# Kernel optimization log

Measured on AMD Instinct MI355X. Metric: run time of the kernel, lower is better.

Reference implementation:

```python
import jax, jax.numpy as jnp
import numpy as np


def setup_inputs() -> dict:
    key = jax.random.key(0)
    k1, k2, k3, k4 = jax.random.split(key, 4)
    B, IN, OUT, S = 8192, 2048, 3072, 8
    scale = 1.0 / (IN ** 0.5)
    x = jax.random.normal(k1, (B, IN), dtype=jnp.float32)
    subject_ids = jax.random.randint(k2, (B,), 0, S, dtype=jnp.int64)
    weights = jax.random.normal(k3, (S, IN, OUT), dtype=jnp.float32) * scale
    bias = jax.random.normal(k4, (S, OUT), dtype=jnp.float32) * scale
    return {"x": x, "subject_ids": subject_ids, "weights": weights, "bias": bias}


def reference(x, subject_ids, weights, bias):
    # Math: out[b] = x[b] @ weights[subject_ids[b]] + bias[subject_ids[b]]
    # Avoid materializing the [B, in, out] gathered weight tensor:
    # contract via a one-hot subject selector instead (same math).
    S = weights.shape[0]
    onehot = jax.nn.one_hot(subject_ids, S, dtype=x.dtype)  # [B, S]
    # [B,d] x [S,d,o] x [B,S] -> [B,o]; intermediate is at most [B,S,o]
    out = jnp.einsum('bd,sdo,bs->bo', x, weights, onehot)
    out = out + bias[subject_ids]  # [B, out]
    return out
```

## Files before the change

kernel.cpp:

```cpp
#include <hip/hip_runtime.h>
#include <hip/hip_bf16.h>
#include <stdint.h>

#define B_ROWS 8192
#define K_DIM  2048
#define N_DIM  3072
#define S_NUM  8

#define BM 256
#define BN 256
#define BK 64
#define NT (K_DIM / BK)
#define MAX_T256 40

#define BMF 128
#define BNF 128
#define BKF 32
#define NKF (K_DIM / BKF)
#define MAX_TILES 72
#define LDA 40
#define LDB 40

typedef __bf16 bf16x8 __attribute__((ext_vector_type(8)));
typedef float  f32x4  __attribute__((ext_vector_type(4)));
typedef unsigned int   u32x4 __attribute__((ext_vector_type(4)));
typedef unsigned short u16x8 __attribute__((ext_vector_type(8)));

#define WS_CNT    0
#define WS_OFFS   256
#define WS_T256S  512
#define WS_T256M  768
#define WS_TILES  1024
#define WS_TILEM  1536
#define WS_RANK   4096
#define WS_PERM   36864
#define WS_XPERM  262144
#define WS_WT     34865152
#define WS_NEED   135528448ULL

__device__ __forceinline__ unsigned int f2bf_pk(float lo, float hi) {
#if __has_builtin(__builtin_amdgcn_cvt_pk_bf16_f32)
    typedef __bf16 bf16x2_t __attribute__((ext_vector_type(2)));
    bf16x2_t v = __builtin_amdgcn_cvt_pk_bf16_f32(lo, hi);
    return __builtin_bit_cast(unsigned int, v);
#else
    unsigned int a = __builtin_bit_cast(unsigned int, lo);
    unsigned int b = __builtin_bit_cast(unsigned int, hi);
    a += 0x7FFFu + ((a >> 16) & 1u);
    b += 0x7FFFu + ((b >> 16) & 1u);
    return (a >> 16) | (b & 0xFFFF0000u);
#endif
}

__device__ __forceinline__ void gl_lds16(const void* g, void* l) {
    __builtin_amdgcn_global_load_lds(
        (const __attribute__((address_space(1))) void*)g,
        (__attribute__((address_space(3))) void*)l, 16, 0, 0);
}

__global__ void zero_cnt_kernel(int* __restrict__ cnt) {
    if (threadIdx.x < S_NUM) cnt[threadIdx.x] = 0;
}

__global__ void bucket_kernel(const int* __restrict__ ids,
                              int* __restrict__ cnt,
                              unsigned short* __restrict__ perm,
                              int* __restrict__ rank) {
    const int b = blockIdx.x * blockDim.x + threadIdx.x;
    const int lane = threadIdx.x & 63;
    const int s = ids[b];
    #pragma unroll
    for (int sub = 0; sub < S_NUM; ++sub) {
        unsigned long long m = __ballot(s == sub);
        if (s == sub) {
            int prefix = __popcll(m & ((1ull << lane) - 1ull));
            int leader = __ffsll((unsigned long long)m) - 1;
            int base = 0;
            if (lane == leader) base = atomicAdd(&cnt[sub], __popcll(m));
            base = __shfl(base, leader);
            perm[sub * B_ROWS + base + prefix] = (unsigned short)b;
            rank[b] = base + prefix;
        }
    }
}

__global__ void plan_kernel(const int* __restrict__ cnt, int* __restrict__ offs,
                            int* __restrict__ t256s, int* __restrict__ t256m,
                            int* __restrict__ tfs, int* __restrict__ tfm) {
    if (threadIdx.x == 0 && blockIdx.x == 0) {
        int t = 0, tf = 0, o = 0;
        for (int s = 0; s < S_NUM; ++s) {
            offs[s] = o; o += cnt[s];
            for (int m0 = 0; m0 < cnt[s]; m0 += BM)  { t256s[t] = s; t256m[t] = m0; ++t; }
            for (int m0 = 0; m0 < cnt[s]; m0 += BMF) { tfs[tf] = s;  tfm[tf] = m0;  ++tf; }
        }
        for (; t < MAX_T256; ++t)    { t256s[t] = -1; t256m[t] = 0; }
        for (; tf < MAX_TILES; ++tf) { tfs[tf]  = -1; tfm[tf]  = 0; }
    }
}

__global__ void convert_x_kernel(const float* __restrict__ x,
                                 const int* __restrict__ ids,
                                 const int* __restrict__ rank,
                                 const int* __restrict__ offs,
                                 unsigned short* __restrict__ xq) {
    const int b = blockIdx.x;
    const int dst = offs[ids[b]] + rank[b];
    const float* src = x + (size_t)b * K_DIM + threadIdx.x * 8;
    f32x4 v0 = *(const f32x4*)(src + 0);
    f32x4 v1 = *(const f32x4*)(src + 4);
    u32x4 p = { f2bf_pk(v0[0], v0[1]), f2bf_pk(v0[2], v0[3]),
                f2bf_pk(v1[0], v1[1]), f2bf_pk(v1[2], v1[3]) };
    *(u32x4*)(xq + (size_t)dst * K_DIM + threadIdx.x * 8) = p;
}

#define TW_LD 136
__global__ void convert_w_kernel(const float* __restrict__ w,
                                 unsigned short* __restrict__ wt) {
    const int kt = blockIdx.x, nt = blockIdx.y, s = blockIdx.z;
    __shared__ __align__(16) unsigned short lds[32 * TW_LD];

    const int tid = threadIdx.x;
    {
        const int k = tid >> 3;
        const int nseg = tid & 7;
        const float* src = w + ((size_t)s * K_DIM + kt * 32 + k) * N_DIM
                             + nt * 128 + nseg * 16;
        f32x4 v0 = *(const f32x4*)(src + 0);
        f32x4 v1 = *(const f32x4*)(src + 4);
        f32x4 v2 = *(const f32x4*)(src + 8);
        f32x4 v3 = *(const f32x4*)(src + 12);
        u32x4 p0 = { f2bf_pk(v0[0], v0[1]), f2bf_pk(v0[2], v0[3]),
                     f2bf_pk(v1[0], v1[1]), f2bf_pk(v1[2], v1[3]) };
        u32x4 p1 = { f2bf_pk(v2[0], v2[1]), f2bf_pk(v2[2], v2[3]),
                     f2bf_pk(v3[0], v3[1]), f2bf_pk(v3[2], v3[3]) };
        *(u32x4*)&lds[k * TW_LD + nseg * 16 + 0] = p0;
        *(u32x4*)&lds[k * TW_LD + nseg * 16 + 8] = p1;
    }
    __syncthreads();
    {
        const int n = tid >> 1;
        const int half = tid & 1;
        u16x8 o0, o1;
        #pragma unroll
        for (int j = 0; j < 8; ++j) {
            o0[j] = lds[(half * 16 + j) * TW_LD + n];
            o1[j] = lds[(half * 16 + 8 + j) * TW_LD + n];
        }
        unsigned short* dst = wt + ((size_t)s * N_DIM + nt * 128 + n) * K_DIM
                                 + kt * 32 + half * 16;
        *(u16x8*)(dst + 0) = o0;
        *(u16x8*)(dst + 8) = o1;
    }
}

__global__ __launch_bounds__(512, 2)
void gemm256_kernel(const unsigned short* __restrict__ xq,
                    const unsigned short* __restrict__ wt,
                    const float* __restrict__ bias,
                    const int* __restrict__ cnt,
                    const int* __restrict__ offs,
                    const int* __restrict__ tile_s,
                    const int* __restrict__ tile_m,
                    const unsigned short* __restrict__ perm,
                    float* __restrict__ out) {
    const int s = tile_s[blockIdx.x];
    if (s < 0) return;
    const int row0 = tile_m[blockIdx.x];
    const int rows = min(BM, cnt[s] - row0);
    const int n0   = blockIdx.y * BN;

    __shared__ __align__(16) char smem[131072 + 1024];
    int* prow = (int*)(smem + 131072);

    const int tid = threadIdx.x;
    if (tid < BM) {
        int rr = (tid < rows) ? tid : (rows - 1);
        prow[tid] = (int)perm[s * B_ROWS + row0 + rr];
    }

    const int lane = tid & 63;
    const int w    = tid >> 6;
    const int wr   = w >> 2;
    const int wc   = w & 3;
    const int l15  = lane & 15;
    const int quad = lane >> 4;

    const int srow  = w * 8 + (lane >> 3);
    const int sperm = ((lane & 7) ^ (lane >> 3)) << 3;
    const int rowA0 = offs[s] + row0;
    const unsigned short* aSrc = xq + (size_t)(rowA0 + srow) * K_DIM + sperm;
    const unsigned short* bSrc = wt + ((size_t)s * N_DIM + n0 + srow) * K_DIM + sperm;
    char* const aDst = smem + w * 1024;
    char* const bDst = smem + 65536 + w * 1024;

    auto stageA = [&](int half, int tt, int bb) {
        int ttc = (tt < NT) ? tt : (NT - 1);
        const unsigned short* g = aSrc + (size_t)half * (128 * K_DIM) + ttc * BK;
        char* d = aDst + (bb * 2 + half) * 16384;
        gl_lds16(g, d);
        gl_lds16(g + 64 * K_DIM, d + 8192);
    };
    auto stageB = [&](int half, int tt, int bb) {
        int ttc = (tt < NT) ? tt : (NT - 1);
        const unsigned short* g = bSrc + (size_t)half * (128 * K_DIM) + ttc * BK;
        char* d = bDst + (bb * 2 + half) * 16384;
        gl_lds16(g, d);
        gl_lds16(g + 64 * K_DIM, d + 8192);
    };

    bf16x8 af[4][2], bfr[2][2];
    auto ldsA = [&](int mh, int bb) {
        const char* base = smem + (bb * 2 + wr) * 16384;
        #pragma unroll
        for (int mt = 0; mt < 4; ++mt) {
            const int row = mh * 64 + mt * 16 + l15;
            #pragma unroll
            for (int kk = 0; kk < 2; ++kk) {
                const int kb = ((kk * 4 + quad) ^ (l15 & 7)) << 4;
                af[mt][kk] = *(const bf16x8*)(base + row * 128 + kb);
            }
        }
    };
    auto ldsB = [&](int nh, int bb) {
        const char* base = smem + 65536 + (bb * 2 + (wc >> 1)) * 16384;
        #pragma unroll
        for (int nt = 0; nt < 2; ++nt) {
            const int row = (wc & 1) * 64 + nh * 32 + nt * 16 + l15;
            #pragma unroll
            for (int kk = 0; kk < 2; ++kk) {
                const int kb = ((kk * 4 + quad) ^ (l15 & 7)) << 4;
                bfr[nt][kk] = *(const bf16x8*)(base + row * 128 + kb);
            }
        }
    };

    f32x4 acc[8][4] = {};
    auto mmac = [&](int mh, int nh) {
        #pragma unroll
        for (int kk = 0; kk < 2; ++kk)
            #pragma unroll
            for (int mt = 0; mt < 4; ++mt)
                #pragma unroll
                for (int nt = 0; nt < 2; ++nt)
                    acc[mh * 4 + mt][nh * 2 + nt] =
                        __builtin_amdgcn_mfma_f32_16x16x32_bf16(
                            af[mt][kk], bfr[nt][kk],
                            acc[mh * 4 + mt][nh * 2 + nt], 0, 0, 0);
    };

    stageA(0, 0, 0); stageA(1, 0, 0);
    stageB(0, 0, 0); stageB(1, 0, 0);
    stageB(0, 1, 1);
    asm volatile("s_waitcnt vmcnt(2)" ::: "memory");
    __builtin_amdgcn_s_barrier();

    for (int T = 0; T < NT; ++T) {
        const int bb = T & 1, nb = bb ^ 1;
        ldsA(0, bb); ldsB(0, bb);
        stageB(1, T + 1, nb);
        __builtin_amdgcn_s_barrier();
        __builtin_amdgcn_s_setprio(1);
        mmac(0, 0);
        __builtin_amdgcn_s_setprio(0);
        __builtin_amdgcn_s_barrier();
        ldsA(1, bb);
        stageA(0, T + 1, nb);
        __builtin_amdgcn_s_barrier();
        __builtin_amdgcn_s_setprio(1);
        mmac(1, 0);
        __builtin_amdgcn_s_setprio(0);
        __builtin_amdgcn_s_barrier();
        ldsB(1, bb);
        stageA(1, T + 1, nb);
        __builtin_amdgcn_s_barrier();
        __builtin_amdgcn_s_setprio(1);
        mmac(1, 1);
        __builtin_amdgcn_s_setprio(0);
        __builtin_amdgcn_s_barrier();
        ldsA(0, bb);
        stageB(0, T + 2, bb);
        asm volatile("s_waitcnt vmcnt(2)" ::: "memory");
        __builtin_amdgcn_s_barrier();
        __builtin_amdgcn_s_setprio(1);
        mmac(0, 1);
        __builtin_amdgcn_s_setprio(0);
        __builtin_amdgcn_s_barrier();
    }

    asm volatile("s_waitcnt vmcnt(0)" ::: "memory");

    float bvals[4];
    #pragma unroll
    for (int nt = 0; nt < 4; ++nt)
        bvals[nt] = bias[s * N_DIM + n0 + wc * 64 + nt * 16 + l15];

    #pragma unroll
    for (int mt = 0; mt < 8; ++mt) {
        #pragma unroll
        for (int r = 0; r < 4; ++r) {
            const int rl = wr * 128 + mt * 16 + quad * 4 + r;
            if (rl < rows) {
                float* op = out + (size_t)prow[rl] * N_DIM + n0 + wc * 64 + l15;
                #pragma unroll
                for (int nt = 0; nt < 4; ++nt)
                    op[nt * 16] = acc[mt][nt][r] + bvals[nt];
            }
        }
    }
}

__global__ __launch_bounds__(256, 3)
void subject_gemm_fb(const float* __restrict__ x,
                     const float* __restrict__ w,
                     const float* __restrict__ bias,
                     const int* __restrict__ cnt,
                     const int* __restrict__ tile_s,
                     const int* __restrict__ tile_m,
                     const unsigned short* __restrict__ perm,
                     float* __restrict__ out) {
    const int s = tile_s[blockIdx.x];
    if (s < 0) return;
    const int row0 = tile_m[blockIdx.x];
    const int rows = min(BMF, cnt[s] - row0);
    const int n0   = blockIdx.y * BNF;

    __shared__ __align__(16) unsigned short sA[BMF * LDA];
    __shared__ __align__(16) unsigned short sB[BNF * LDB];
    __shared__ int prow[BMF];

    const int tid = threadIdx.x;
    if (tid < BMF) {
        int rr = (tid < rows) ? tid : (rows - 1);
        prow[tid] = (int)perm[s * B_ROWS + row0 + rr];
    }
    __syncthreads();

    const int ar = tid >> 1;
    const int ah = tid & 1;
    const float* xp = x + (size_t)prow[ar] * K_DIM + ah * 16;
    const int bn  = tid & 127;
    const int bk2 = tid >> 7;
    const float* wp = w + (size_t)s * ((size_t)K_DIM * N_DIM)
                        + (size_t)(bk2 * 16) * N_DIM + (n0 + bn);

    const int lane = tid & 63;
    const int wid  = tid >> 6;
    const int wm   = (wid >> 1) * 64;
    const int wn   = (wid & 1) * 64;
    const int l15  = lane & 15;
    const int quad = lane >> 4;

    f32x4 acc[4][4] = {};
    f32x4 a0, a1, a2, a3;
    float bv[16];
    {
        a0 = *(const f32x4*)(xp + 0);  a1 = *(const f32x4*)(xp + 4);
        a2 = *(const f32x4*)(xp + 8);  a3 = *(const f32x4*)(xp + 12);
        #pragma unroll
        for (int i = 0; i < 16; ++i) bv[i] = wp[(size_t)i * N_DIM];
    }

    for (int ks = 0; ks < NKF; ++ks) {
        u32x4 pa0 = { f2bf_pk(a0[0],a0[1]), f2bf_pk(a0[2],a0[3]),
                      f2bf_pk(a1[0],a1[1]), f2bf_pk(a1[2],a1[3]) };
        u32x4 pa1 = { f2bf_pk(a2[0],a2[1]), f2bf_pk(a2[2],a2[3]),
                      f2bf_pk(a3[0],a3[1]), f2bf_pk(a3[2],a3[3]) };
        u32x4 pb0 = { f2bf_pk(bv[0],bv[1]),   f2bf_pk(bv[2],bv[3]),
                      f2bf_pk(bv[4],bv[5]),   f2bf_pk(bv[6],bv[7]) };
        u32x4 pb1 = { f2bf_pk(bv[8],bv[9]),   f2bf_pk(bv[10],bv[11]),
                      f2bf_pk(bv[12],bv[13]), f2bf_pk(bv[14],bv[15]) };

        __syncthreads();
        *(u32x4*)&sA[ar * LDA + ah * 16 + 0] = pa0;
        *(u32x4*)&sA[ar * LDA + ah * 16 + 8] = pa1;
        *(u32x4*)&sB[bn * LDB + bk2 * 16 + 0] = pb0;
        *(u32x4*)&sB[bn * LDB + bk2 * 16 + 8] = pb1;
        __syncthreads();

        if (ks + 1 < NKF) {
            const float* xq2 = xp + (ks + 1) * BKF;
            a0 = *(const f32x4*)(xq2 + 0);  a1 = *(const f32x4*)(xq2 + 4);
            a2 = *(const f32x4*)(xq2 + 8);  a3 = *(const f32x4*)(xq2 + 12);
            const float* wq = wp + (size_t)((ks + 1) * BKF) * N_DIM;
            #pragma unroll
            for (int i = 0; i < 16; ++i) bv[i] = wq[(size_t)i * N_DIM];
        }

        bf16x8 af[4], bfr[4];
        #pragma unroll
        for (int mt = 0; mt < 4; ++mt)
            af[mt] = *(const bf16x8*)&sA[(wm + mt * 16 + l15) * LDA + quad * 8];
        #pragma unroll
        for (int nt = 0; nt < 4; ++nt)
            bfr[nt] = *(const bf16x8*)&sB[(wn + nt * 16 + l15) * LDB + quad * 8];

        #pragma unroll
        for (int mt = 0; mt < 4; ++mt)
            #pragma unroll
            for (int nt = 0; nt < 4; ++nt)
                acc[mt][nt] = __builtin_amdgcn_mfma_f32_16x16x32_bf16(
                    af[mt], bfr[nt], acc[mt][nt], 0, 0, 0);
    }

    float bvals[4];
    #pragma unroll
    for (int nt = 0; nt < 4; ++nt)
        bvals[nt] = bias[s * N_DIM + n0 + wn + nt * 16 + l15];
    #pragma unroll
    for (int mt = 0; mt < 4; ++mt) {
        #pragma unroll
        for (int r = 0; r < 4; ++r) {
            int rl = wm + mt * 16 + quad * 4 + r;
            if (rl < rows) {
                float* op = out + (size_t)prow[rl] * N_DIM + n0 + wn + l15;
                #pragma unroll
                for (int nt = 0; nt < 4; ++nt)
                    op[nt * 16] = acc[mt][nt][r] + bvals[nt];
            }
        }
    }
}

extern "C" void kernel_launch(void* const* d_in, const int* in_sizes, int n_in,
                              void* d_out, int out_size, void* d_ws, size_t ws_size,
                              hipStream_t stream) {
    const float* x    = (const float*)d_in[0];
    const int*   sid  = (const int*)d_in[1];
    const float* w    = (const float*)d_in[2];
    const float* bias = (const float*)d_in[3];
    float* out = (float*)d_out;

    char* ws = (char*)d_ws;
    int* cnt    = (int*)(ws + WS_CNT);
    int* offs   = (int*)(ws + WS_OFFS);
    int* t256s  = (int*)(ws + WS_T256S);
    int* t256m  = (int*)(ws + WS_T256M);
    int* tfs    = (int*)(ws + WS_TILES);
    int* tfm    = (int*)(ws + WS_TILEM);
    int* rank   = (int*)(ws + WS_RANK);
    unsigned short* perm = (unsigned short*)(ws + WS_PERM);

    hipLaunchKernelGGL(zero_cnt_kernel, dim3(1), dim3(64), 0, stream, cnt);
    hipLaunchKernelGGL(bucket_kernel, dim3(B_ROWS / 256), dim3(256), 0, stream,
                       sid, cnt, perm, rank);
    hipLaunchKernelGGL(plan_kernel, dim3(1), dim3(64), 0, stream,
                       cnt, offs, t256s, t256m, tfs, tfm);

    if (ws_size >= WS_NEED) {
        unsigned short* xq = (unsigned short*)(ws + WS_XPERM);
        unsigned short* wt = (unsigned short*)(ws + WS_WT);
        hipLaunchKernelGGL(convert_x_kernel, dim3(B_ROWS), dim3(256), 0, stream,
                           x, sid, rank, offs, xq);
        hipLaunchKernelGGL(convert_w_kernel, dim3(K_DIM / 32, N_DIM / 128, S_NUM),
                           dim3(256), 0, stream, w, wt);
        dim3 grid(MAX_T256, N_DIM / BN);
        hipLaunchKernelGGL(gemm256_kernel, grid, dim3(512), 0, stream,
                           xq, wt, bias, cnt, offs, t256s, t256m, perm, out);
    } else {
        dim3 grid(MAX_TILES, N_DIM / BNF);
        hipLaunchKernelGGL(subject_gemm_fb, grid, dim3(256), 0, stream,
                           x, w, bias, cnt, tfs, tfm, perm, out);
    }
}
```

Baseline: 519.6 us.

## Fuse bucketing prep kernels and reorder GEMM inner loop to double-buffer B fragments

Three small setup kernels (zero counts, bucket rows by subject, build tile plan) are merged into one single-block kernel that counts with LDS atomics, removing two launches and the global atomics. The GEMM main loop is reordered so B fragments for both N-halves sit in separate register sets (bf0/bf1). This lets each quarter step reuse the fragments already loaded and drops one A reload per K-tile. The cost is extra VGPR pressure and a serial single-block prep pass over all 8192 rows.

```diff
diff --git a/kernel.cpp b/kernel.cpp
--- a/kernel.cpp
+++ b/kernel.cpp
@@ -58,41 +58,43 @@
         (__attribute__((address_space(3))) void*)l, 16, 0, 0);
 }
 
-__global__ void zero_cnt_kernel(int* __restrict__ cnt) {
-    if (threadIdx.x < S_NUM) cnt[threadIdx.x] = 0;
-}
-
-__global__ void bucket_kernel(const int* __restrict__ ids,
-                              int* __restrict__ cnt,
-                              unsigned short* __restrict__ perm,
-                              int* __restrict__ rank) {
-    const int b = blockIdx.x * blockDim.x + threadIdx.x;
-    const int lane = threadIdx.x & 63;
-    const int s = ids[b];
+__global__ __launch_bounds__(1024)
+void prep_kernel(const int* __restrict__ ids,
+                 int* __restrict__ cnt, int* __restrict__ offs,
+                 int* __restrict__ t256s, int* __restrict__ t256m,
+                 int* __restrict__ tfs, int* __restrict__ tfm,
+                 unsigned short* __restrict__ perm, int* __restrict__ rank) {
+    __shared__ int lcnt[S_NUM];
+    const int tid = threadIdx.x;
+    if (tid < S_NUM) lcnt[tid] = 0;
+    __syncthreads();
+    const int lane = tid & 63;
     #pragma unroll
-    for (int sub = 0; sub < S_NUM; ++sub) {
-        unsigned long long m = __ballot(s == sub);
-        if (s == sub) {
-            int prefix = __popcll(m & ((1ull << lane) - 1ull));
-            int leader = __ffsll((unsigned long long)m) - 1;
-            int base = 0;
-            if (lane == leader) base = atomicAdd(&cnt[sub], __popcll(m));
-            base = __shfl(base, leader);
-            perm[sub * B_ROWS + base + prefix] = (unsigned short)b;
-            rank[b] = base + prefix;
-        }
-    }
-}
-
-__global__ void plan_kernel(const int* __restrict__ cnt, int* __restrict__ offs,
-                            int* __restrict__ t256s, int* __restrict__ t256m,
-                            int* __restrict__ tfs, int* __restrict__ tfm) {
-    if (threadIdx.x == 0 && blockIdx.x == 0) {
+    for (int c = 0; c < B_ROWS / 1024; ++c) {
+        const int b = c * 1024 + tid;
+        const int s = ids[b];
+        #pragma unroll
+        for (int sub = 0; sub < S_NUM; ++sub) {
+            unsigned long long m = __ballot(s == sub);
+            if (s == sub) {
+                int prefix = __popcll(m & ((1ull << lane) - 1ull));
+                int leader = __ffsll((unsigned long long)m) - 1;
+                int base = 0;
+                if (lane == leader) base = atomicAdd(&lcnt[sub], __popcll(m));
+                base = __shfl(base, leader);
+                perm[sub * B_ROWS + base + prefix] = (unsigned short)b;
+                rank[b] = base + prefix;
+            }
+        }
+    }
+    __syncthreads();
+    if (tid == 0) {
         int t = 0, tf = 0, o = 0;
-        for (int s = 0; s < S_NUM; ++s) {
-            offs[s] = o; o += cnt[s];
-            for (int m0 = 0; m0 < cnt[s]; m0 += BM)  { t256s[t] = s; t256m[t] = m0; ++t; }
-            for (int m0 = 0; m0 < cnt[s]; m0 += BMF) { tfs[tf] = s;  tfm[tf] = m0;  ++tf; }
+        for (int s2 = 0; s2 < S_NUM; ++s2) {
+            const int c2 = lcnt[s2];
+            cnt[s2] = c2; offs[s2] = o; o += c2;
+            for (int m0 = 0; m0 < c2; m0 += BM)  { t256s[t] = s2; t256m[t] = m0; ++t; }
+            for (int m0 = 0; m0 < c2; m0 += BMF) { tfs[tf] = s2;  tfm[tf] = m0;  ++tf; }
         }
         for (; t < MAX_T256; ++t)    { t256s[t] = -1; t256m[t] = 0; }
         for (; tf < MAX_TILES; ++tf) { tfs[tf]  = -1; tfm[tf]  = 0; }
@@ -209,7 +211,7 @@
         gl_lds16(g + 64 * K_DIM, d + 8192);
     };
 
-    bf16x8 af[4][2], bfr[2][2];
+    bf16x8 af[4][2], bf0[2][2], bf1[2][2];
     auto ldsA = [&](int mh, int bb) {
         const char* base = smem + (bb * 2 + wr) * 16384;
         #pragma unroll
@@ -222,7 +224,7 @@
             }
         }
     };
-    auto ldsB = [&](int nh, int bb) {
+    auto ldsB = [&](int nh, int bb, bf16x8 (*dst)[2]) {
         const char* base = smem + 65536 + (bb * 2 + (wc >> 1)) * 16384;
         #pragma unroll
         for (int nt = 0; nt < 2; ++nt) {
@@ -230,13 +232,13 @@
             #pragma unroll
             for (int kk = 0; kk < 2; ++kk) {
                 const int kb = ((kk * 4 + quad) ^ (l15 & 7)) << 4;
-                bfr[nt][kk] = *(const bf16x8*)(base + row * 128 + kb);
+                dst[nt][kk] = *(const bf16x8*)(base + row * 128 + kb);
             }
         }
     };
 
     f32x4 acc[8][4] = {};
-    auto mmac = [&](int mh, int nh) {
+    auto mmac = [&](bf16x8 (*b)[2], int mh, int nh) {
         #pragma unroll
         for (int kk = 0; kk < 2; ++kk)
             #pragma unroll
@@ -245,7 +247,7 @@
                 for (int nt = 0; nt < 2; ++nt)
                     acc[mh * 4 + mt][nh * 2 + nt] =
                         __builtin_amdgcn_mfma_f32_16x16x32_bf16(
-                            af[mt][kk], bfr[nt][kk],
+                            af[mt][kk], b[nt][kk],
                             acc[mh * 4 + mt][nh * 2 + nt], 0, 0, 0);
     };
 
@@ -257,33 +259,32 @@
 
     for (int T = 0; T < NT; ++T) {
         const int bb = T & 1, nb = bb ^ 1;
-        ldsA(0, bb); ldsB(0, bb);
+        ldsA(0, bb); ldsB(0, bb, bf0);
         stageB(1, T + 1, nb);
         __builtin_amdgcn_s_barrier();
         __builtin_amdgcn_s_setprio(1);
-        mmac(0, 0);
+        mmac(bf0, 0, 0);
         __builtin_amdgcn_s_setprio(0);
         __builtin_amdgcn_s_barrier();
+        ldsB(1, bb, bf1);
+        stageA(0, T + 1, nb);
+        __builtin_amdgcn_s_barrier();
+        __builtin_amdgcn_s_setprio(1);
+        mmac(bf1, 0, 1);
+        __builtin_amdgcn_s_setprio(0);
+        __builtin_amdgcn_s_barrier();
         ldsA(1, bb);
-        stageA(0, T + 1, nb);
+        stageA(1, T + 1, nb);
         __builtin_amdgcn_s_barrier();
         __builtin_amdgcn_s_setprio(1);
-        mmac(1, 0);
+        mmac(bf1, 1, 1);
         __builtin_amdgcn_s_setprio(0);
         __builtin_amdgcn_s_barrier();
-        ldsB(1, bb);
-        stageA(1, T + 1, nb);
-        __builtin_amdgcn_s_barrier();
-        __builtin_amdgcn_s_setprio(1);
-        mmac(1, 1);
-        __builtin_amdgcn_s_setprio(0);
-        __builtin_amdgcn_s_barrier();
-        ldsA(0, bb);
         stageB(0, T + 2, bb);
         asm volatile("s_waitcnt vmcnt(2)" ::: "memory");
         __builtin_amdgcn_s_barrier();
         __builtin_amdgcn_s_setprio(1);
-        mmac(0, 1);
+        mmac(bf0, 1, 0);
         __builtin_amdgcn_s_setprio(0);
         __builtin_amdgcn_s_barrier();
     }
@@ -441,11 +442,8 @@
     int* rank   = (int*)(ws + WS_RANK);
     unsigned short* perm = (unsigned short*)(ws + WS_PERM);
 
-    hipLaunchKernelGGL(zero_cnt_kernel, dim3(1), dim3(64), 0, stream, cnt);
-    hipLaunchKernelGGL(bucket_kernel, dim3(B_ROWS / 256), dim3(256), 0, stream,
-                       sid, cnt, perm, rank);
-    hipLaunchKernelGGL(plan_kernel, dim3(1), dim3(64), 0, stream,
-                       cnt, offs, t256s, t256m, tfs, tfm);
+    hipLaunchKernelGGL(prep_kernel, dim3(1), dim3(1024), 0, stream,
+                       sid, cnt, offs, t256s, t256m, tfs, tfm, perm, rank);
 
     if (ws_size >= WS_NEED) {
         unsigned short* xq = (unsigned short*)(ws + WS_XPERM);
```

Result: no change. 514.9 us (-0.9%).
